# Kernel tuning notes

Hardware: AMD Instinct MI355X
Metric: run time of the kernel (lower is better)

Reference implementation:

```python
import jax, jax.numpy as jnp
import numpy as np

B, CIN, HIN, WIN = 8192, 16, 6, 6
FM = 64                      # feature_maps
DK = FM // 2                 # 32
DV = FM // 2                 # 32
NH = FM // 2                 # 32 heads -> dkh = dvh = 1
OUT_CH = 5
HID = 128


def _conv2d(x, w, b, stride=1):
    # x: NCHW, w: OIHW, VALID padding (padding=(k-1)//2 = 0 for k=2)
    y = jax.lax.conv_general_dilated(
        x, w, window_strides=(stride, stride), padding='VALID',
        dimension_numbers=('NCHW', 'OIHW', 'NCHW'))
    return y + b[None, :, None, None]


def setup_inputs() -> dict:
    key = jax.random.key(0)
    ks = jax.random.split(key, 13)
    s = 0.1  # small init scale keeps softmax logits well-conditioned
    return {
        'x':      jax.random.normal(ks[0], (B, CIN, HIN, WIN), jnp.float32),
        # AugmentedConv: conv_out (out_channels - dv), qkv conv (2dk+dv), attn 1x1
        'conv_w': jax.random.normal(ks[1], (FM - DV, CIN, 2, 2), jnp.float32) * s,
        'conv_b': jax.random.normal(ks[2], (FM - DV,), jnp.float32) * s,
        'qkv_w':  jax.random.normal(ks[3], (2 * DK + DV, CIN, 2, 2), jnp.float32) * s,
        'qkv_b':  jax.random.normal(ks[4], (2 * DK + DV,), jnp.float32) * s,
        'attn_w': jax.random.normal(ks[5], (DV, DV, 1, 1), jnp.float32) * s,
        'attn_b': jax.random.normal(ks[6], (DV,), jnp.float32) * s,
        # DoubleDense: fm*5*5 -> hid -> hid//2 -> out
        'w1': jax.random.normal(ks[7], (HID, FM * 5 * 5), jnp.float32) * s,
        'b1': jax.random.normal(ks[8], (HID,), jnp.float32) * s,
        'w2': jax.random.normal(ks[9], (HID // 2, HID), jnp.float32) * s,
        'b2': jax.random.normal(ks[10], (HID // 2,), jnp.float32) * s,
        'w3': jax.random.normal(ks[11], (OUT_CH, HID // 2), jnp.float32) * s,
        'b3': jax.random.normal(ks[12], (OUT_CH,), jnp.float32) * s,
    }


def _forward(x, conv_w, conv_b, qkv_w, qkv_b, attn_w, attn_b, w1, b1, w2, b2, w3, b3):
    # ---- AugmentedConv ----
    conv_out = _conv2d(x, conv_w, conv_b)            # [B, FM-DV, 5, 5]
    qkv = _conv2d(x, qkv_w, qkv_b)                   # [B, 2DK+DV, 5, 5]
    b, _, h, w = qkv.shape
    q, k, v = jnp.split(qkv, [DK, 2 * DK], axis=1)
    dkh = DK // NH
    q = q * (dkh ** -0.5)
    flat_q = q.reshape(b, NH, dkh, h * w)            # [B, Nh, dkh, HW]
    flat_k = k.reshape(b, NH, dkh, h * w)
    flat_v = v.reshape(b, NH, DV // NH, h * w)
    # logits = q^T k over head-dim: [B, Nh, HW, HW]
    logits = jnp.einsum('bndi,bndj->bnij', flat_q, flat_k)
    weights = jax.nn.softmax(logits, axis=-1)
    # attn = weights @ v^T -> [B, Nh, HW, dvh]
    attn = jnp.einsum('bnij,bnjd->bnid', weights, flat_v.transpose(0, 1, 3, 2))
    # faithful to torch: raw reshape (B, Nh, dvh, H, W) then combine heads
    attn = attn.reshape(b, NH, DV // NH, h, w).reshape(b, DV, h, w)
    attn = _conv2d(attn, attn_w, attn_b)             # 1x1 conv
    y = jnp.concatenate([conv_out, attn], axis=1)    # [B, FM, 5, 5]
    # ---- ReLU + DoubleDense ----
    y = jax.nn.relu(y).reshape(b, -1)                # [B, FM*25]
    y = jax.nn.relu(y @ w1.T + b1)
    y = jax.nn.relu(y @ w2.T + b2)
    return y @ w3.T + b3                             # [B, OUT_CH]


def reference(x, conv_w, conv_b, qkv_w, qkv_b, attn_w, attn_b, w1, b1, w2, b2, w3, b3):
    return _forward(x, conv_w, conv_b, qkv_w, qkv_b, attn_w, attn_b,
                    w1, b1, w2, b2, w3, b3)
```

## Files before the change

kernel.cpp:

```cpp
#include <hip/hip_runtime.h>
#include <hip/hip_bf16.h>
#include <cstdint>
#include <cstddef>


typedef __attribute__((ext_vector_type(4))) float f32x4;
typedef __attribute__((ext_vector_type(2))) float f32x2;
typedef __attribute__((ext_vector_type(8))) __bf16 bf16x8;
typedef __attribute__((ext_vector_type(4))) __bf16 bf16x4;

#define LOG2E 1.4426950408889634f

__device__ __forceinline__ float fast_exp2(float x) {
#if __has_builtin(__builtin_amdgcn_exp2f)
  return __builtin_amdgcn_exp2f(x);
#else
  return __expf(x * 0.6931471805599453f);
#endif
}

__device__ __forceinline__ f32x4 mfma16(bf16x8 a, bf16x8 b, f32x4 c) {
  return __builtin_amdgcn_mfma_f32_16x16x32_bf16(a, b, c, 0, 0, 0);
}

__global__ __launch_bounds__(64) void prep_small(
    const float* __restrict__ conv_w, const float* __restrict__ conv_b,
    const float* __restrict__ qkv_w,  const float* __restrict__ qkv_b,
    const float* __restrict__ attn_w,
    __hip_bfloat16* __restrict__ wqb, float* __restrict__ biasb,
    __hip_bfloat16* __restrict__ wab) {
  const int t = threadIdx.x, tb = blockIdx.x;
  if (tb < 16) {
#pragma unroll
    for (int j = 0; j < 8; ++j) {
      int i = tb * 512 + j * 64 + t;
      float w = (i < 2048) ? conv_w[i] : qkv_w[i - 2048];
      if (i >= 4096 && i < 6144) w *= LOG2E;
      wqb[i] = __float2bfloat16(w);
    }
  } else {
#pragma unroll
    for (int j = 0; j < 16; ++j) wab[j * 64 + t] = __float2bfloat16(attn_w[j * 64 + t]);
    for (int i = t; i < 128; i += 64) {
      float b = (i < 32) ? conv_b[i] : qkv_b[i - 32];
      if (i >= 64 && i < 96) b *= LOG2E;
      biasb[i] = b;
    }
  }
}

__global__ __launch_bounds__(128) void k1(
    const float* __restrict__ x,
    const float* __restrict__ biasb,
    const __hip_bfloat16* __restrict__ wqb,
    const __hip_bfloat16* __restrict__ wab, const float* __restrict__ attn_b,
    const float* __restrict__ w1, const float* __restrict__ w2,
    __hip_bfloat16* __restrict__ act,
    __hip_bfloat16* __restrict__ w1bp, __hip_bfloat16* __restrict__ w2b) {
  const int t = threadIdx.x & 63;
  const int wv = threadIdx.x >> 6;

  __shared__ __align__(16) char lds_raw[2 * 7168];
  char* my = lds_raw + wv * 7168;

  if (blockIdx.x >= 4096) {
    const int u = (blockIdx.x - 4096) * 2 + wv;
    if (u < 128) {
      float* rowf = (float*)my;
      const float* wr = w1 + u * 1600;
#pragma unroll
      for (int j = 0; j < 25; ++j) rowf[j * 64 + t] = wr[j * 64 + t];
      __hip_bfloat16* wo = w1bp + u * 1600;
#pragma unroll
      for (int j = 0; j < 25; ++j) {
        wo[j * 64 + t] = __float2bfloat16(rowf[t * 25 + j]);
      }
    } else if (u < 132) {
#pragma unroll
      for (int j = 0; j < 32; ++j) {
        int i = (u - 128) * 2048 + j * 64 + t;
        w2b[i] = __float2bfloat16(w2[i]);
      }
    }
    return;
  }

  const int l15 = t & 15, quad = t >> 4;
  const int b = blockIdx.x * 2 + wv;
  __bf16* xs  = (__bf16*)my;
  __bf16* as_ = (__bf16*)my;
  __bf16* qs  = (__bf16*)(my + 1600);

  const float* xb = x + (size_t)b * 576;
#pragma unroll
  for (int i = 0; i < 9; ++i) {
    int f = t + i * 64;
    xs[f] = __float2bfloat16(xb[f]);
  }

  bf16x8 bfr[8][2];
#pragma unroll
  for (int nt = 0; nt < 8; ++nt)
#pragma unroll
    for (int ks = 0; ks < 2; ++ks)
      bfr[nt][ks] = *(const bf16x8*)((const __bf16*)wqb + (nt * 16 + l15) * 64 + ks * 32 + quad * 8);
  float bias[8];
#pragma unroll
  for (int nt = 0; nt < 8; ++nt) bias[nt] = biasb[nt * 16 + l15];

#pragma unroll
  for (int mt = 0; mt < 2; ++mt) {
    int row = mt * 16 + l15;
    int pos = row < 24 ? row : 24;
    int ii = pos / 5, jj = pos - ii * 5;
    const __bf16* xp = xs + ii * 6 + jj;
    bf16x8 af[2];
#pragma unroll
    for (int ks = 0; ks < 2; ++ks) {
      const __bf16* p0 = xp + (ks * 8 + quad * 2) * 36;
      bf16x8 a;
      a[0] = p0[0];  a[1] = p0[1];  a[2] = p0[6];  a[3] = p0[7];
      a[4] = p0[36]; a[5] = p0[37]; a[6] = p0[42]; a[7] = p0[43];
      af[ks] = a;
    }
    f32x4 acc[8];
#pragma unroll
    for (int nt = 0; nt < 8; ++nt) acc[nt] = (f32x4){0.f, 0.f, 0.f, 0.f};
#pragma unroll
    for (int ks = 0; ks < 2; ++ks)
#pragma unroll
      for (int nt = 0; nt < 8; ++nt)
        acc[nt] = mfma16(af[ks], bfr[nt][ks], acc[nt]);

#pragma unroll
    for (int r = 0; r < 4; ++r) {
      int orow = mt * 16 + quad * 4 + r;
      if (orow < 25) {
#pragma unroll
        for (int nt = 0; nt < 8; ++nt) {
          float v = acc[nt][r] + bias[nt];
          if (nt < 2) {
            act[((size_t)b * 25 + orow) * 64 + nt * 16 + l15] =
                __float2bfloat16(fmaxf(v, 0.f));
          } else {
            qs[((nt - 2) * 16 + l15) * 28 + orow] = __float2bfloat16(v);
          }
        }
      }
    }
  }

  {
    const int n = t & 31, half = t >> 5;
    const __bf16* qp = qs + n * 28;
    const __bf16* kp = qs + (32 + n) * 28;
    const __bf16* vp = qs + (64 + n) * 28;
    f32x2 kl2[12], vv2[12];
    float kl24, vv24;
#pragma unroll
    for (int c4 = 0; c4 < 6; ++c4) {
      bf16x4 bb = *(const bf16x4*)(kp + c4 * 4);
      bf16x4 cc = *(const bf16x4*)(vp + c4 * 4);
      kl2[c4 * 2]     = (f32x2){(float)bb[0], (float)bb[1]};
      kl2[c4 * 2 + 1] = (f32x2){(float)bb[2], (float)bb[3]};
      vv2[c4 * 2]     = (f32x2){(float)cc[0], (float)cc[1]};
      vv2[c4 * 2 + 1] = (f32x2){(float)cc[2], (float)cc[3]};
    }
    kl24 = (float)kp[24]; vv24 = (float)vp[24];

    const int i0 = half * 12;
    float qv[13];
    {
      const __bf16* qbase = qp + i0;
      bf16x4 q0 = *(const bf16x4*)(qbase);
      bf16x4 q1 = *(const bf16x4*)(qbase + 4);
      bf16x4 q2 = *(const bf16x4*)(qbase + 8);
#pragma unroll
      for (int z = 0; z < 4; ++z) {
        qv[z] = (float)q0[z]; qv[4 + z] = (float)q1[z]; qv[8 + z] = (float)q2[z];
      }
      qv[12] = (float)qbase[12];
    }

#pragma unroll
    for (int z = 0; z < 13; ++z) {
      const float qi = qv[z];
      const f32x2 qi2 = {qi, qi};
      f32x2 sA = {0.f, 0.f}, sB = {0.f, 0.f};
      f32x2 oA = {0.f, 0.f}, oB = {0.f, 0.f};
      float s4 = 0.f, o4 = 0.f;
#pragma unroll
      for (int p = 0; p < 6; ++p) {
        f32x2 mA = qi2 * kl2[p];
        f32x2 mB = qi2 * kl2[p + 6];
        f32x2 eA = {fast_exp2(mA.x), fast_exp2(mA.y)};
        f32x2 eB = {fast_exp2(mB.x), fast_exp2(mB.y)};
        sA += eA;
        sB += eB;
        oA = eA * vv2[p] + oA;
        oB = eB * vv2[p + 6] + oB;
      }
      {
        float e = fast_exp2(qi * kl24);
        s4 += e;
        o4 = __builtin_fmaf(e, vv24, o4);
      }
      float ss = ((sA.x + sA.y) + (sB.x + sB.y)) + s4;
      float oo = ((oA.x + oA.y) + (oB.x + oB.y)) + o4;
      as_[(i0 + z) * 32 + n] = __float2bfloat16(oo * __builtin_amdgcn_rcpf(ss));
    }
  }

  {
    bf16x8 bw[2]; float ab[2];
#pragma unroll
    for (int nt2 = 0; nt2 < 2; ++nt2) {
      int n = nt2 * 16 + l15;
      bw[nt2] = *(const bf16x8*)((const __bf16*)wab + n * 32 + quad * 8);
      ab[nt2] = attn_b[n];
    }
#pragma unroll
    for (int mt = 0; mt < 2; ++mt) {
      int row = mt * 16 + l15;
      int rc = row < 24 ? row : 24;
      bf16x8 af = *(const bf16x8*)(as_ + rc * 32 + quad * 8);
      f32x4 acc[2];
#pragma unroll
      for (int nt2 = 0; nt2 < 2; ++nt2)
        acc[nt2] = mfma16(af, bw[nt2], (f32x4){0.f, 0.f, 0.f, 0.f});
#pragma unroll
      for (int r = 0; r < 4; ++r) {
        int orow = mt * 16 + quad * 4 + r;
        if (orow < 25) {
#pragma unroll
          for (int nt2 = 0; nt2 < 2; ++nt2)
            act[((size_t)b * 25 + orow) * 64 + 32 + nt2 * 16 + l15] =
                __float2bfloat16(fmaxf(acc[nt2][r] + ab[nt2], 0.f));
        }
      }
    }
  }
}

__global__ __launch_bounds__(512) void k2(
    const __hip_bfloat16* __restrict__ act,
    const __hip_bfloat16* __restrict__ w1bp, const float* __restrict__ b1,
    const __hip_bfloat16* __restrict__ w2b, const float* __restrict__ b2,
    const float* __restrict__ w3, const float* __restrict__ b3,
    float* __restrict__ out) {
  const int t = threadIdx.x;
  const int lane = t & 63;
  const int wave = t >> 6;
  const int wm = wave >> 2;
  const int wn = wave & 3;
  const int l15 = lane & 15;
  const int quad = lane >> 4;
  const int b0 = blockIdx.x * 32;

  __shared__ __hip_bfloat16 C1s[32 * 136];
  __shared__ __hip_bfloat16 C2s[32 * 72];

  f32x4 acc0 = {0.f, 0.f, 0.f, 0.f};
  f32x4 acc1 = {0.f, 0.f, 0.f, 0.f};
  const __bf16* aptr  = (const __bf16*)act + (size_t)(b0 + wm * 16 + l15) * 1600 + quad * 8;
  const __bf16* bptr0 = (const __bf16*)w1bp + (size_t)(wn * 32 + l15) * 1600 + quad * 8;
  const __bf16* bptr1 = bptr0 + 16 * 1600;
#pragma unroll 5
  for (int k0 = 0; k0 < 1600; k0 += 32) {
    bf16x8 av  = *(const bf16x8*)(aptr + k0);
    bf16x8 bv0 = *(const bf16x8*)(bptr0 + k0);
    bf16x8 bv1 = *(const bf16x8*)(bptr1 + k0);
    acc0 = mfma16(av, bv0, acc0);
    acc1 = mfma16(av, bv1, acc1);
  }
  {
    const int col0 = wn * 32 + l15;
    const float bias0 = b1[col0];
    const float bias1 = b1[col0 + 16];
#pragma unroll
    for (int r = 0; r < 4; ++r) {
      const int row = wm * 16 + quad * 4 + r;
      C1s[row * 136 + col0]      = __float2bfloat16(fmaxf(acc0[r] + bias0, 0.f));
      C1s[row * 136 + col0 + 16] = __float2bfloat16(fmaxf(acc1[r] + bias1, 0.f));
    }
  }
  __syncthreads();

  f32x4 acc2 = {0.f, 0.f, 0.f, 0.f};
  {
    const __bf16* aL = (const __bf16*)C1s + (wm * 16 + l15) * 136 + quad * 8;
    const __bf16* bL = (const __bf16*)w2b + (wn * 16 + l15) * 128 + quad * 8;
#pragma unroll
    for (int k0 = 0; k0 < 128; k0 += 32)
      acc2 = mfma16(*(const bf16x8*)(aL + k0), *(const bf16x8*)(bL + k0), acc2);
  }
  {
    const int col = wn * 16 + l15;
    const float bias = b2[col];
#pragma unroll
    for (int r = 0; r < 4; ++r) {
      const int row = wm * 16 + quad * 4 + r;
      C2s[row * 72 + col] = __float2bfloat16(fmaxf(acc2[r] + bias, 0.f));
    }
  }
  __syncthreads();

  if (t < 160) {
    const int row = t / 5;
    const int oc = t - row * 5;
    float s = b3[oc];
#pragma unroll
    for (int k = 0; k < 64; ++k)
      s += __bfloat162float(C2s[row * 72 + k]) * w3[oc * 64 + k];
    out[(size_t)(b0 + row) * 5 + oc] = s;
  }
}

extern "C" void kernel_launch(void* const* d_in, const int* in_sizes, int n_in,
                              void* d_out, int out_size, void* d_ws, size_t ws_size,
                              hipStream_t stream) {
  const float* x      = (const float*)d_in[0];
  const float* conv_w = (const float*)d_in[1];
  const float* conv_b = (const float*)d_in[2];
  const float* qkv_w  = (const float*)d_in[3];
  const float* qkv_b  = (const float*)d_in[4];
  const float* attn_w = (const float*)d_in[5];
  const float* attn_b = (const float*)d_in[6];
  const float* w1 = (const float*)d_in[7];
  const float* b1 = (const float*)d_in[8];
  const float* w2 = (const float*)d_in[9];
  const float* b2 = (const float*)d_in[10];
  const float* w3 = (const float*)d_in[11];
  const float* b3 = (const float*)d_in[12];
  float* out = (float*)d_out;

  char* ws = (char*)d_ws;
  __hip_bfloat16* act   = (__hip_bfloat16*)ws;
  __hip_bfloat16* w1bp  = (__hip_bfloat16*)(ws + 26214400);
  __hip_bfloat16* w2b   = (__hip_bfloat16*)(ws + 26624000);
  __hip_bfloat16* wqb   = (__hip_bfloat16*)(ws + 26640384);
  float*          biasb = (float*)(ws + 26656768);
  __hip_bfloat16* wab   = (__hip_bfloat16*)(ws + 26657280);

  prep_small<<<dim3(17), dim3(64), 0, stream>>>(conv_w, conv_b, qkv_w, qkv_b, attn_w,
                                                wqb, biasb, wab);
  k1<<<dim3(4096 + 66), dim3(128), 0, stream>>>(x, biasb, wqb, wab, attn_b,
                                                w1, w2, act, w1bp, w2b);
  k2<<<dim3(256), dim3(512), 0, stream>>>(act, w1bp, b1, w2b, b2, w3, b3, out);
}
```

Baseline: 161.0 us.

## Fuse augmented-conv stage into dense MLP kernel, keeping activations in LDS

Result: faster. 148.3 us (median of 3 runs) (-7.9%).

```diff
diff --git a/kernel.cpp b/kernel.cpp
--- a/kernel.cpp
+++ b/kernel.cpp
@@ -10,6 +10,10 @@
 typedef __attribute__((ext_vector_type(4))) __bf16 bf16x4;
 
 #define LOG2E 1.4426950408889634f
+#define ACT_STRIDE 1608
+#define ACT_LDS_BYTES (32 * ACT_STRIDE * 2)
+#define SCRATCH_OFF ACT_LDS_BYTES
+#define LDS_TOTAL (ACT_LDS_BYTES + 8 * 7168)
 
 __device__ __forceinline__ float fast_exp2(float x) {
 #if __has_builtin(__builtin_amdgcn_exp2f)
@@ -23,12 +27,14 @@
   return __builtin_amdgcn_mfma_f32_16x16x32_bf16(a, b, c, 0, 0, 0);
 }
 
-__global__ __launch_bounds__(64) void prep_small(
+__global__ __launch_bounds__(64) void prep(
     const float* __restrict__ conv_w, const float* __restrict__ conv_b,
     const float* __restrict__ qkv_w,  const float* __restrict__ qkv_b,
     const float* __restrict__ attn_w,
+    const float* __restrict__ w1, const float* __restrict__ w2,
     __hip_bfloat16* __restrict__ wqb, float* __restrict__ biasb,
-    __hip_bfloat16* __restrict__ wab) {
+    __hip_bfloat16* __restrict__ wab,
+    __hip_bfloat16* __restrict__ w1bp, __hip_bfloat16* __restrict__ w2b) {
   const int t = threadIdx.x, tb = blockIdx.x;
   if (tb < 16) {
 #pragma unroll
@@ -38,7 +44,7 @@
       if (i >= 4096 && i < 6144) w *= LOG2E;
       wqb[i] = __float2bfloat16(w);
     }
-  } else {
+  } else if (tb == 16) {
 #pragma unroll
     for (int j = 0; j < 16; ++j) wab[j * 64 + t] = __float2bfloat16(attn_w[j * 64 + t]);
     for (int i = t; i < 128; i += 64) {
@@ -46,232 +52,235 @@
       if (i >= 64 && i < 96) b *= LOG2E;
       biasb[i] = b;
     }
-  }
-}
-
-__global__ __launch_bounds__(128) void k1(
+  } else if (tb < 145) {
+    const int u = tb - 17;
+    __shared__ float rowf[1600];
+    const float* wr = w1 + u * 1600;
+#pragma unroll
+    for (int j = 0; j < 25; ++j) rowf[j * 64 + t] = wr[j * 64 + t];
+    __hip_bfloat16* wo = w1bp + u * 1600;
+#pragma unroll
+    for (int j = 0; j < 25; ++j) {
+      wo[j * 64 + t] = __float2bfloat16(rowf[t * 25 + j]);
+    }
+  } else {
+#pragma unroll
+    for (int j = 0; j < 64; ++j) {
+      int i = (tb - 145) * 4096 + j * 64 + t;
+      w2b[i] = __float2bfloat16(w2[i]);
+    }
+  }
+}
+
+__global__ __launch_bounds__(512) void kf(
     const float* __restrict__ x,
     const float* __restrict__ biasb,
     const __hip_bfloat16* __restrict__ wqb,
     const __hip_bfloat16* __restrict__ wab, const float* __restrict__ attn_b,
-    const float* __restrict__ w1, const float* __restrict__ w2,
-    __hip_bfloat16* __restrict__ act,
-    __hip_bfloat16* __restrict__ w1bp, __hip_bfloat16* __restrict__ w2b) {
-  const int t = threadIdx.x & 63;
-  const int wv = threadIdx.x >> 6;
-
-  __shared__ __align__(16) char lds_raw[2 * 7168];
-  char* my = lds_raw + wv * 7168;
-
-  if (blockIdx.x >= 4096) {
-    const int u = (blockIdx.x - 4096) * 2 + wv;
-    if (u < 128) {
-      float* rowf = (float*)my;
-      const float* wr = w1 + u * 1600;
-#pragma unroll
-      for (int j = 0; j < 25; ++j) rowf[j * 64 + t] = wr[j * 64 + t];
-      __hip_bfloat16* wo = w1bp + u * 1600;
-#pragma unroll
-      for (int j = 0; j < 25; ++j) {
-        wo[j * 64 + t] = __float2bfloat16(rowf[t * 25 + j]);
-      }
-    } else if (u < 132) {
-#pragma unroll
-      for (int j = 0; j < 32; ++j) {
-        int i = (u - 128) * 2048 + j * 64 + t;
-        w2b[i] = __float2bfloat16(w2[i]);
-      }
-    }
-    return;
-  }
-
-  const int l15 = t & 15, quad = t >> 4;
-  const int b = blockIdx.x * 2 + wv;
-  __bf16* xs  = (__bf16*)my;
-  __bf16* as_ = (__bf16*)my;
-  __bf16* qs  = (__bf16*)(my + 1600);
-
-  const float* xb = x + (size_t)b * 576;
-#pragma unroll
-  for (int i = 0; i < 9; ++i) {
-    int f = t + i * 64;
-    xs[f] = __float2bfloat16(xb[f]);
-  }
-
-  bf16x8 bfr[8][2];
-#pragma unroll
-  for (int nt = 0; nt < 8; ++nt)
-#pragma unroll
-    for (int ks = 0; ks < 2; ++ks)
-      bfr[nt][ks] = *(const bf16x8*)((const __bf16*)wqb + (nt * 16 + l15) * 64 + ks * 32 + quad * 8);
-  float bias[8];
-#pragma unroll
-  for (int nt = 0; nt < 8; ++nt) bias[nt] = biasb[nt * 16 + l15];
-
-#pragma unroll
-  for (int mt = 0; mt < 2; ++mt) {
-    int row = mt * 16 + l15;
-    int pos = row < 24 ? row : 24;
-    int ii = pos / 5, jj = pos - ii * 5;
-    const __bf16* xp = xs + ii * 6 + jj;
-    bf16x8 af[2];
-#pragma unroll
-    for (int ks = 0; ks < 2; ++ks) {
-      const __bf16* p0 = xp + (ks * 8 + quad * 2) * 36;
-      bf16x8 a;
-      a[0] = p0[0];  a[1] = p0[1];  a[2] = p0[6];  a[3] = p0[7];
-      a[4] = p0[36]; a[5] = p0[37]; a[6] = p0[42]; a[7] = p0[43];
-      af[ks] = a;
-    }
-    f32x4 acc[8];
-#pragma unroll
-    for (int nt = 0; nt < 8; ++nt) acc[nt] = (f32x4){0.f, 0.f, 0.f, 0.f};
-#pragma unroll
-    for (int ks = 0; ks < 2; ++ks)
-#pragma unroll
-      for (int nt = 0; nt < 8; ++nt)
-        acc[nt] = mfma16(af[ks], bfr[nt][ks], acc[nt]);
-
-#pragma unroll
-    for (int r = 0; r < 4; ++r) {
-      int orow = mt * 16 + quad * 4 + r;
-      if (orow < 25) {
-#pragma unroll
-        for (int nt = 0; nt < 8; ++nt) {
-          float v = acc[nt][r] + bias[nt];
-          if (nt < 2) {
-            act[((size_t)b * 25 + orow) * 64 + nt * 16 + l15] =
-                __float2bfloat16(fmaxf(v, 0.f));
-          } else {
-            qs[((nt - 2) * 16 + l15) * 28 + orow] = __float2bfloat16(v);
-          }
-        }
-      }
-    }
-  }
-
-  {
-    const int n = t & 31, half = t >> 5;
-    const __bf16* qp = qs + n * 28;
-    const __bf16* kp = qs + (32 + n) * 28;
-    const __bf16* vp = qs + (64 + n) * 28;
-    f32x2 kl2[12], vv2[12];
-    float kl24, vv24;
-#pragma unroll
-    for (int c4 = 0; c4 < 6; ++c4) {
-      bf16x4 bb = *(const bf16x4*)(kp + c4 * 4);
-      bf16x4 cc = *(const bf16x4*)(vp + c4 * 4);
-      kl2[c4 * 2]     = (f32x2){(float)bb[0], (float)bb[1]};
-      kl2[c4 * 2 + 1] = (f32x2){(float)bb[2], (float)bb[3]};
-      vv2[c4 * 2]     = (f32x2){(float)cc[0], (float)cc[1]};
-      vv2[c4 * 2 + 1] = (f32x2){(float)cc[2], (float)cc[3]};
-    }
-    kl24 = (float)kp[24]; vv24 = (float)vp[24];
-
-    const int i0 = half * 12;
-    float qv[13];
-    {
-      const __bf16* qbase = qp + i0;
-      bf16x4 q0 = *(const bf16x4*)(qbase);
-      bf16x4 q1 = *(const bf16x4*)(qbase + 4);
-      bf16x4 q2 = *(const bf16x4*)(qbase + 8);
-#pragma unroll
-      for (int z = 0; z < 4; ++z) {
-        qv[z] = (float)q0[z]; qv[4 + z] = (float)q1[z]; qv[8 + z] = (float)q2[z];
-      }
-      qv[12] = (float)qbase[12];
-    }
-
-#pragma unroll
-    for (int z = 0; z < 13; ++z) {
-      const float qi = qv[z];
-      const f32x2 qi2 = {qi, qi};
-      f32x2 sA = {0.f, 0.f}, sB = {0.f, 0.f};
-      f32x2 oA = {0.f, 0.f}, oB = {0.f, 0.f};
-      float s4 = 0.f, o4 = 0.f;
-#pragma unroll
-      for (int p = 0; p < 6; ++p) {
-        f32x2 mA = qi2 * kl2[p];
-        f32x2 mB = qi2 * kl2[p + 6];
-        f32x2 eA = {fast_exp2(mA.x), fast_exp2(mA.y)};
-        f32x2 eB = {fast_exp2(mB.x), fast_exp2(mB.y)};
-        sA += eA;
-        sB += eB;
-        oA = eA * vv2[p] + oA;
-        oB = eB * vv2[p + 6] + oB;
-      }
-      {
-        float e = fast_exp2(qi * kl24);
-        s4 += e;
-        o4 = __builtin_fmaf(e, vv24, o4);
-      }
-      float ss = ((sA.x + sA.y) + (sB.x + sB.y)) + s4;
-      float oo = ((oA.x + oA.y) + (oB.x + oB.y)) + o4;
-      as_[(i0 + z) * 32 + n] = __float2bfloat16(oo * __builtin_amdgcn_rcpf(ss));
-    }
-  }
-
-  {
-    bf16x8 bw[2]; float ab[2];
-#pragma unroll
-    for (int nt2 = 0; nt2 < 2; ++nt2) {
-      int n = nt2 * 16 + l15;
-      bw[nt2] = *(const bf16x8*)((const __bf16*)wab + n * 32 + quad * 8);
-      ab[nt2] = attn_b[n];
-    }
-#pragma unroll
-    for (int mt = 0; mt < 2; ++mt) {
-      int row = mt * 16 + l15;
-      int rc = row < 24 ? row : 24;
-      bf16x8 af = *(const bf16x8*)(as_ + rc * 32 + quad * 8);
-      f32x4 acc[2];
-#pragma unroll
-      for (int nt2 = 0; nt2 < 2; ++nt2)
-        acc[nt2] = mfma16(af, bw[nt2], (f32x4){0.f, 0.f, 0.f, 0.f});
-#pragma unroll
-      for (int r = 0; r < 4; ++r) {
-        int orow = mt * 16 + quad * 4 + r;
-        if (orow < 25) {
-#pragma unroll
-          for (int nt2 = 0; nt2 < 2; ++nt2)
-            act[((size_t)b * 25 + orow) * 64 + 32 + nt2 * 16 + l15] =
-                __float2bfloat16(fmaxf(acc[nt2][r] + ab[nt2], 0.f));
-        }
-      }
-    }
-  }
-}
-
-__global__ __launch_bounds__(512) void k2(
-    const __hip_bfloat16* __restrict__ act,
     const __hip_bfloat16* __restrict__ w1bp, const float* __restrict__ b1,
     const __hip_bfloat16* __restrict__ w2b, const float* __restrict__ b2,
     const float* __restrict__ w3, const float* __restrict__ b3,
     float* __restrict__ out) {
-  const int t = threadIdx.x;
-  const int lane = t & 63;
-  const int wave = t >> 6;
+  extern __shared__ __align__(16) char lds_all[];
+  const int t = threadIdx.x & 63;
+  const int wv = threadIdx.x >> 6;
+  const int l15 = t & 15, quad = t >> 4;
+
+  __hip_bfloat16* act_lds = (__hip_bfloat16*)lds_all;
+  char* my = lds_all + SCRATCH_OFF + wv * 7168;
+  __bf16* xs  = (__bf16*)my;
+  __bf16* as_ = (__bf16*)my;
+  __bf16* qs  = (__bf16*)(my + 1600);
+
+  bf16x8 bfr[8][2];
+#pragma unroll
+  for (int nt = 0; nt < 8; ++nt)
+#pragma unroll
+    for (int ks = 0; ks < 2; ++ks)
+      bfr[nt][ks] = *(const bf16x8*)((const __bf16*)wqb + (nt * 16 + l15) * 64 + ks * 32 + quad * 8);
+  float bias[8];
+#pragma unroll
+  for (int nt = 0; nt < 8; ++nt) bias[nt] = biasb[nt * 16 + l15];
+  bf16x8 bw[2]; float ab[2];
+#pragma unroll
+  for (int nt2 = 0; nt2 < 2; ++nt2) {
+    int n = nt2 * 16 + l15;
+    bw[nt2] = *(const bf16x8*)((const __bf16*)wab + n * 32 + quad * 8);
+    ab[nt2] = attn_b[n];
+  }
+
+  const int b_base = blockIdx.x * 32 + wv * 4;
+
+  float xr[9];
+  {
+    const float* xb = x + (size_t)b_base * 576;
+#pragma unroll
+    for (int i = 0; i < 9; ++i) xr[i] = xb[t + i * 64];
+  }
+
+  for (int it = 0; it < 4; ++it) {
+    const int rowoff = (wv * 4 + it) * ACT_STRIDE;
+
+#pragma unroll
+    for (int i = 0; i < 9; ++i) xs[t + i * 64] = __float2bfloat16(xr[i]);
+
+#pragma unroll
+    for (int mt = 0; mt < 2; ++mt) {
+      int row = mt * 16 + l15;
+      int pos = row < 24 ? row : 24;
+      int ii = pos / 5, jj = pos - ii * 5;
+      const __bf16* xp = xs + ii * 6 + jj;
+      bf16x8 af[2];
+#pragma unroll
+      for (int ks = 0; ks < 2; ++ks) {
+        const __bf16* p0 = xp + (ks * 8 + quad * 2) * 36;
+        bf16x8 a;
+        a[0] = p0[0];  a[1] = p0[1];  a[2] = p0[6];  a[3] = p0[7];
+        a[4] = p0[36]; a[5] = p0[37]; a[6] = p0[42]; a[7] = p0[43];
+        af[ks] = a;
+      }
+      f32x4 acc[8];
+#pragma unroll
+      for (int nt = 0; nt < 8; ++nt) acc[nt] = (f32x4){0.f, 0.f, 0.f, 0.f};
+#pragma unroll
+      for (int ks = 0; ks < 2; ++ks)
+#pragma unroll
+        for (int nt = 0; nt < 8; ++nt)
+          acc[nt] = mfma16(af[ks], bfr[nt][ks], acc[nt]);
+
+#pragma unroll
+      for (int r = 0; r < 4; ++r) {
+        int orow = mt * 16 + quad * 4 + r;
+        if (orow < 25) {
+#pragma unroll
+          for (int nt = 0; nt < 8; ++nt) {
+            float v = acc[nt][r] + bias[nt];
+            if (nt < 2) {
+              act_lds[rowoff + orow * 64 + nt * 16 + l15] =
+                  __float2bfloat16(fmaxf(v, 0.f));
+            } else {
+              qs[((nt - 2) * 16 + l15) * 28 + orow] = __float2bfloat16(v);
+            }
+          }
+        }
+      }
+    }
+
+    if (it < 3) {
+      const float* xb = x + (size_t)(b_base + it + 1) * 576;
+#pragma unroll
+      for (int i = 0; i < 9; ++i) xr[i] = xb[t + i * 64];
+    }
+
+    {
+      const int n = t & 31, half = t >> 5;
+      const __bf16* qp = qs + n * 28;
+      const __bf16* kp = qs + (32 + n) * 28;
+      const __bf16* vp = qs + (64 + n) * 28;
+      f32x2 kl2[12], vv2[12];
+      float kl24, vv24;
+#pragma unroll
+      for (int c4 = 0; c4 < 6; ++c4) {
+        bf16x4 bb = *(const bf16x4*)(kp + c4 * 4);
+        bf16x4 cc = *(const bf16x4*)(vp + c4 * 4);
+        kl2[c4 * 2]     = (f32x2){(float)bb[0], (float)bb[1]};
+        kl2[c4 * 2 + 1] = (f32x2){(float)bb[2], (float)bb[3]};
+        vv2[c4 * 2]     = (f32x2){(float)cc[0], (float)cc[1]};
+        vv2[c4 * 2 + 1] = (f32x2){(float)cc[2], (float)cc[3]};
+      }
+      kl24 = (float)kp[24]; vv24 = (float)vp[24];
+
+      const int i0 = half * 12;
+      float qv[13];
+      {
+        const __bf16* qbase = qp + i0;
+        bf16x4 q0 = *(const bf16x4*)(qbase);
+        bf16x4 q1 = *(const bf16x4*)(qbase + 4);
+        bf16x4 q2 = *(const bf16x4*)(qbase + 8);
+#pragma unroll
+        for (int z = 0; z < 4; ++z) {
+          qv[z] = (float)q0[z]; qv[4 + z] = (float)q1[z]; qv[8 + z] = (float)q2[z];
+        }
+        qv[12] = (float)qbase[12];
+      }
+
+#pragma unroll
+      for (int z = 0; z < 13; ++z) {
+        const float qi = qv[z];
+        const f32x2 qi2 = {qi, qi};
+        f32x2 sA = {0.f, 0.f}, sB = {0.f, 0.f};
+        f32x2 oA = {0.f, 0.f}, oB = {0.f, 0.f};
+        float s4 = 0.f, o4 = 0.f;
+#pragma unroll
+        for (int p = 0; p < 6; ++p) {
+          f32x2 mA = qi2 * kl2[p];
+          f32x2 mB = qi2 * kl2[p + 6];
+          f32x2 eA = {fast_exp2(mA.x), fast_exp2(mA.y)};
+          f32x2 eB = {fast_exp2(mB.x), fast_exp2(mB.y)};
+          sA += eA;
+          sB += eB;
+          oA = eA * vv2[p] + oA;
+          oB = eB * vv2[p + 6] + oB;
+        }
+        {
+          float e = fast_exp2(qi * kl24);
+          s4 += e;
+          o4 = __builtin_fmaf(e, vv24, o4);
+        }
+        float ss = ((sA.x + sA.y) + (sB.x + sB.y)) + s4;
+        float oo = ((oA.x + oA.y) + (oB.x + oB.y)) + o4;
+        as_[(i0 + z) * 32 + n] = __float2bfloat16(oo * __builtin_amdgcn_rcpf(ss));
+      }
+    }
+
+    {
+#pragma unroll
+      for (int mt = 0; mt < 2; ++mt) {
+        int row = mt * 16 + l15;
+        int rc = row < 24 ? row : 24;
+        bf16x8 af = *(const bf16x8*)(as_ + rc * 32 + quad * 8);
+        f32x4 acc[2];
+#pragma unroll
+        for (int nt2 = 0; nt2 < 2; ++nt2)
+          acc[nt2] = mfma16(af, bw[nt2], (f32x4){0.f, 0.f, 0.f, 0.f});
+#pragma unroll
+        for (int r = 0; r < 4; ++r) {
+          int orow = mt * 16 + quad * 4 + r;
+          if (orow < 25) {
+#pragma unroll
+            for (int nt2 = 0; nt2 < 2; ++nt2)
+              act_lds[rowoff + orow * 64 + 32 + nt2 * 16 + l15] =
+                  __float2bfloat16(fmaxf(acc[nt2][r] + ab[nt2], 0.f));
+          }
+        }
+      }
+    }
+  }
+
+  __syncthreads();
+
+  const int wave = threadIdx.x >> 6;
   const int wm = wave >> 2;
   const int wn = wave & 3;
-  const int l15 = lane & 15;
-  const int quad = lane >> 4;
   const int b0 = blockIdx.x * 32;
 
-  __shared__ __hip_bfloat16 C1s[32 * 136];
-  __shared__ __hip_bfloat16 C2s[32 * 72];
+  __hip_bfloat16* C1s = (__hip_bfloat16*)(lds_all + SCRATCH_OFF);
+  __hip_bfloat16* C2s = (__hip_bfloat16*)(lds_all + SCRATCH_OFF + 8704);
 
   f32x4 acc0 = {0.f, 0.f, 0.f, 0.f};
   f32x4 acc1 = {0.f, 0.f, 0.f, 0.f};
-  const __bf16* aptr  = (const __bf16*)act + (size_t)(b0 + wm * 16 + l15) * 1600 + quad * 8;
-  const __bf16* bptr0 = (const __bf16*)w1bp + (size_t)(wn * 32 + l15) * 1600 + quad * 8;
-  const __bf16* bptr1 = bptr0 + 16 * 1600;
+  {
+    const __bf16* aL    = (const __bf16*)act_lds + (wm * 16 + l15) * ACT_STRIDE + quad * 8;
+    const __bf16* bptr0 = (const __bf16*)w1bp + (size_t)(wn * 32 + l15) * 1600 + quad * 8;
+    const __bf16* bptr1 = bptr0 + 16 * 1600;
 #pragma unroll 5
-  for (int k0 = 0; k0 < 1600; k0 += 32) {
-    bf16x8 av  = *(const bf16x8*)(aptr + k0);
-    bf16x8 bv0 = *(const bf16x8*)(bptr0 + k0);
-    bf16x8 bv1 = *(const bf16x8*)(bptr1 + k0);
-    acc0 = mfma16(av, bv0, acc0);
-    acc1 = mfma16(av, bv1, acc1);
+    for (int k0 = 0; k0 < 1600; k0 += 32) {
+      bf16x8 av  = *(const bf16x8*)(aL + k0);
+      bf16x8 bv0 = *(const bf16x8*)(bptr0 + k0);
+      bf16x8 bv1 = *(const bf16x8*)(bptr1 + k0);
+      acc0 = mfma16(av, bv0, acc0);
+      acc1 = mfma16(av, bv1, acc1);
+    }
   }
   {
     const int col0 = wn * 32 + l15;
@@ -305,9 +314,9 @@
   }
   __syncthreads();
 
-  if (t < 160) {
-    const int row = t / 5;
-    const int oc = t - row * 5;
+  if (threadIdx.x < 160) {
+    const int row = threadIdx.x / 5;
+    const int oc = threadIdx.x - row * 5;
     float s = b3[oc];
 #pragma unroll
     for (int k = 0; k < 64; ++k)
@@ -335,16 +344,17 @@
   float* out = (float*)d_out;
 
   char* ws = (char*)d_ws;
-  __hip_bfloat16* act   = (__hip_bfloat16*)ws;
-  __hip_bfloat16* w1bp  = (__hip_bfloat16*)(ws + 26214400);
-  __hip_bfloat16* w2b   = (__hip_bfloat16*)(ws + 26624000);
-  __hip_bfloat16* wqb   = (__hip_bfloat16*)(ws + 26640384);
-  float*          biasb = (float*)(ws + 26656768);
-  __hip_bfloat16* wab   = (__hip_bfloat16*)(ws + 26657280);
-
-  prep_small<<<dim3(17), dim3(64), 0, stream>>>(conv_w, conv_b, qkv_w, qkv_b, attn_w,
-                                                wqb, biasb, wab);
-  k1<<<dim3(4096 + 66), dim3(128), 0, stream>>>(x, biasb, wqb, wab, attn_b,
-                                                w1, w2, act, w1bp, w2b);
-  k2<<<dim3(256), dim3(512), 0, stream>>>(act, w1bp, b1, w2b, b2, w3, b3, out);
-}
+  __hip_bfloat16* w1bp  = (__hip_bfloat16*)ws;
+  __hip_bfloat16* w2b   = (__hip_bfloat16*)(ws + 409600);
+  __hip_bfloat16* wqb   = (__hip_bfloat16*)(ws + 425984);
+  float*          biasb = (float*)(ws + 442368);
+  __hip_bfloat16* wab   = (__hip_bfloat16*)(ws + 442880);
+
+  hipFuncSetAttribute(reinterpret_cast<const void*>(kf),
+                      hipFuncAttributeMaxDynamicSharedMemorySize, LDS_TOTAL);
+
+  prep<<<dim3(147), dim3(64), 0, stream>>>(conv_w, conv_b, qkv_w, qkv_b, attn_w,
+                                           w1, w2, wqb, biasb, wab, w1bp, w2b);
+  kf<<<dim3(256), dim3(512), LDS_TOTAL, stream>>>(x, biasb, wqb, wab, attn_b,
+                                                  w1bp, b1, w2b, b2, w3, b3, out);
+}
```
